# Kernel tuning notes

Measured on AMD Instinct MI355X. Metric: run time of the kernel, lower is better.

## Reference

```python
import jax, jax.numpy as jnp
import numpy as np

N, INSIZE, K, D = 512, 512, 64, 16


def setup_inputs() -> dict:
    key = jax.random.key(0)
    k1, k2, k3 = jax.random.split(key, 3)
    x = jax.random.normal(k1, (N, INSIZE), dtype=jnp.float32)
    W = jax.random.normal(k2, (K * D, INSIZE), dtype=jnp.float32) * (1.0 / np.sqrt(INSIZE))
    b = jax.random.normal(k3, (K * D,), dtype=jnp.float32) * 0.01
    return {"x": x, "W": W, "b": b}


def reference(x, W, b):
    # Linear: [N, insize] -> [N, K*D] -> [N, K, D]
    feat = (x @ W.T + b).reshape(-1, K, D)
    n = feat.shape[0]
    # Pairwise L1 distance over D: norm[i, k, j] = sum_d |feat[i,k,d] - feat[j,k,d]|
    # feature [N,K,D,1] vs feature_ [1,K,D,N] in the original broadcast
    diff = jnp.abs(feat[:, :, :, None] - jnp.transpose(feat, (1, 2, 0))[None])  # [N,K,D,N]
    norm = jnp.sum(diff, axis=2)  # [N,K,N]
    # Eraser: suppress self-similarity on the diagonal with a large penalty
    eraser = jnp.eye(n, dtype=feat.dtype)[:, None, :]  # [N,1,N]
    c_b = jnp.exp(-(norm + eraser * 1e6))
    o_b = jnp.sum(c_b, axis=2)  # [N,K]
    return jnp.concatenate((x, o_b), axis=1)  # [N, insize+K]
```

## Files before the change

### kernel.cpp

```cpp
#include <hip/hip_runtime.h>

#define NPTS 512
#define INS  512
#define KDIM 64
#define DDIM 16
#define CDIM (KDIM*DDIM)
#define OUTC (INS + KDIM)

typedef __attribute__((ext_vector_type(4))) float f32x4;
typedef __attribute__((ext_vector_type(8))) short short8v;
typedef __attribute__((ext_vector_type(4))) unsigned short u16x4;
typedef __attribute__((ext_vector_type(8))) unsigned short u16x8;

__device__ __forceinline__ float exp2_fast(float x) {
    return __builtin_amdgcn_exp2f(x);
}

__device__ __forceinline__ unsigned short f2bf_rne(float f) {
    unsigned u = __float_as_uint(f);
    u += 0x7FFF + ((u >> 16) & 1);
    return (unsigned short)(u >> 16);
}
__device__ __forceinline__ float bf2f(unsigned short h) {
    return __uint_as_float(((unsigned)h) << 16);
}

__global__ __launch_bounds__(256) void convert_kernel(
    const float* __restrict__ x, const float* __restrict__ W,
    float* __restrict__ out,
    unsigned short* __restrict__ xh, unsigned short* __restrict__ xl,
    unsigned short* __restrict__ wh, unsigned short* __restrict__ wl)
{
    const int b = blockIdx.x;
    const int tid = threadIdx.x;
    if (b < 768) {
        const int gid = b * 256 + tid;
        const float4* src;
        unsigned short *dh, *dl;
        int idx;
        if (gid < NPTS * INS / 4) {
            src = (const float4*)x; idx = gid; dh = xh; dl = xl;
        } else {
            src = (const float4*)W; idx = gid - NPTS * INS / 4; dh = wh; dl = wl;
        }
        float4 v = src[idx];
        u16x4 hv, lv;
        hv[0] = f2bf_rne(v.x); lv[0] = f2bf_rne(v.x - bf2f(hv[0]));
        hv[1] = f2bf_rne(v.y); lv[1] = f2bf_rne(v.y - bf2f(hv[1]));
        hv[2] = f2bf_rne(v.z); lv[2] = f2bf_rne(v.z - bf2f(hv[2]));
        hv[3] = f2bf_rne(v.w); lv[3] = f2bf_rne(v.w - bf2f(hv[3]));
        *(u16x4*)&dh[idx * 4] = hv;
        *(u16x4*)&dl[idx * 4] = lv;
    } else {
        const int idx = (b - 768) * 256 + tid;
        const int i  = idx >> 7;
        const int j4 = idx & 127;
        ((float4*)out)[i * (OUTC / 4) + j4] = ((const float4*)x)[i * (INS / 4) + j4];
    }
}

#define BM 32
#define BN 64
#define BK 32
#define LDK 40

__global__ __launch_bounds__(256) void gemm_mfma_kernel(
    const unsigned short* __restrict__ xh, const unsigned short* __restrict__ xl,
    const unsigned short* __restrict__ wh, const unsigned short* __restrict__ wl,
    const float* __restrict__ bias,
    float* __restrict__ featT)
{
    __shared__ unsigned short Ah[BM * LDK], Al[BM * LDK];
    __shared__ unsigned short Bh[BN * LDK], Bl[BN * LDK];

    const int tid   = threadIdx.x;
    const int cbase = blockIdx.x * BN;
    const int ibase = blockIdx.y * BM;

    const int lane = tid & 63;
    const int wv   = tid >> 6;
    const int wm   = wv >> 1;
    const int wn   = wv & 1;

    const int arow = (tid & 127) >> 2;
    const int brow = tid >> 2;
    const int kg   = tid & 3;
    const bool doA = (tid < 128);
    const size_t gA0 = (size_t)(ibase + arow) * INS + kg * 8;
    const size_t gB0 = (size_t)(cbase + brow) * INS + kg * 8;
    const int aloff = arow * LDK + kg * 8;
    const int bloff = brow * LDK + kg * 8;

    const int frow = lane & 15;
    const int fg   = lane >> 4;
    const int aoff = (wm * 16 + frow) * LDK + fg * 8;
    const int boff = (wn * 32 + frow) * LDK + fg * 8;

    f32x4 acc[2] = {};

    u16x8 rah, ral, rbh, rbl;
    if (doA) { rah = *(const u16x8*)&xh[gA0]; ral = *(const u16x8*)&xl[gA0]; }
    rbh = *(const u16x8*)&wh[gB0];
    rbl = *(const u16x8*)&wl[gB0];

    for (int kt = 0; kt < INS / BK; ++kt) {
        __syncthreads();
        if (doA) { *(u16x8*)&Ah[aloff] = rah; *(u16x8*)&Al[aloff] = ral; }
        *(u16x8*)&Bh[bloff] = rbh;
        *(u16x8*)&Bl[bloff] = rbl;
        __syncthreads();
        if (kt + 1 < INS / BK) {
            const size_t o = (size_t)(kt + 1) * BK;
            if (doA) { rah = *(const u16x8*)&xh[gA0 + o]; ral = *(const u16x8*)&xl[gA0 + o]; }
            rbh = *(const u16x8*)&wh[gB0 + o];
            rbl = *(const u16x8*)&wl[gB0 + o];
        }

        short8v av_h = *(const short8v*)&Ah[aoff];
        short8v av_l = *(const short8v*)&Al[aoff];
        #pragma unroll
        for (int n = 0; n < 2; ++n) {
            short8v bv_h = *(const short8v*)&Bh[boff + n * 16 * LDK];
            short8v bv_l = *(const short8v*)&Bl[boff + n * 16 * LDK];
            acc[n] = __builtin_amdgcn_mfma_f32_16x16x32_bf16(av_h, bv_h, acc[n], 0, 0, 0);
            acc[n] = __builtin_amdgcn_mfma_f32_16x16x32_bf16(av_h, bv_l, acc[n], 0, 0, 0);
            acc[n] = __builtin_amdgcn_mfma_f32_16x16x32_bf16(av_l, bv_h, acc[n], 0, 0, 0);
        }
    }

    const float LOG2E = 1.4426950408889634f;
    const int r0 = (lane >> 4) * 4;
    const int i0 = ibase + wm * 16 + r0;
    #pragma unroll
    for (int n = 0; n < 2; ++n) {
        const int c  = cbase + wn * 32 + n * 16 + (lane & 15);
        const float bv = bias[c];
        const int kk = c >> 4;
        const int d  = c & 15;
        float* dst = featT + (size_t)kk * NPTS * DDIM + d;
        #pragma unroll
        for (int r = 0; r < 4; ++r) {
            dst[(size_t)(i0 + r) * DDIM] = (acc[n][r] + bv) * LOG2E;
        }
    }
}

__global__ __launch_bounds__(1024, 4) void pairwise_kernel(
    const float* __restrict__ f, float* __restrict__ out)
{
    const int k     = blockIdx.x;
    const int itile = blockIdx.y;

    __shared__ float part[16][128];

    const int tid  = threadIdx.x;
    const int lane = tid & 63;
    const int wv   = __builtin_amdgcn_readfirstlane(tid >> 6);
    const int i0   = itile * 128 + lane;
    const int i1   = i0 + 64;

    float fi0[16], fi1[16];
    {
        const float4* p0 = (const float4*)(f + ((size_t)k * NPTS + i0) * DDIM);
        const float4* p1 = (const float4*)(f + ((size_t)k * NPTS + i1) * DDIM);
        #pragma unroll
        for (int q = 0; q < 4; ++q) {
            float4 a = p0[q];
            fi0[q * 4 + 0] = a.x; fi0[q * 4 + 1] = a.y;
            fi0[q * 4 + 2] = a.z; fi0[q * 4 + 3] = a.w;
            float4 b = p1[q];
            fi1[q * 4 + 0] = b.x; fi1[q * 4 + 1] = b.y;
            fi1[q * 4 + 2] = b.z; fi1[q * 4 + 3] = b.w;
        }
    }

    const float* __restrict__ jrow = f + ((size_t)k * NPTS + wv * 32) * DDIM;

    float acc0 = 0.f, acc1 = 0.f;
    #pragma unroll 2
    for (int jj = 0; jj < 32; ++jj) {
        const float* p = jrow + jj * DDIM;
        float4 q0 = *(const float4*)(p);
        float4 q1 = *(const float4*)(p + 4);
        float4 q2 = *(const float4*)(p + 8);
        float4 q3 = *(const float4*)(p + 12);
        {
            float a0 = fabsf(fi0[0]  - q0.x) + fabsf(fi0[1]  - q0.y)
                     + fabsf(fi0[2]  - q0.z) + fabsf(fi0[3]  - q0.w);
            float a1 = fabsf(fi0[4]  - q1.x) + fabsf(fi0[5]  - q1.y)
                     + fabsf(fi0[6]  - q1.z) + fabsf(fi0[7]  - q1.w);
            float a2 = fabsf(fi0[8]  - q2.x) + fabsf(fi0[9]  - q2.y)
                     + fabsf(fi0[10] - q2.z) + fabsf(fi0[11] - q2.w);
            float a3 = fabsf(fi0[12] - q3.x) + fabsf(fi0[13] - q3.y)
                     + fabsf(fi0[14] - q3.z) + fabsf(fi0[15] - q3.w);
            acc0 += exp2_fast(-((a0 + a1) + (a2 + a3)));
        }
        {
            float b0 = fabsf(fi1[0]  - q0.x) + fabsf(fi1[1]  - q0.y)
                     + fabsf(fi1[2]  - q0.z) + fabsf(fi1[3]  - q0.w);
            float b1 = fabsf(fi1[4]  - q1.x) + fabsf(fi1[5]  - q1.y)
                     + fabsf(fi1[6]  - q1.z) + fabsf(fi1[7]  - q1.w);
            float b2 = fabsf(fi1[8]  - q2.x) + fabsf(fi1[9]  - q2.y)
                     + fabsf(fi1[10] - q2.z) + fabsf(fi1[11] - q2.w);
            float b3 = fabsf(fi1[12] - q3.x) + fabsf(fi1[13] - q3.y)
                     + fabsf(fi1[14] - q3.z) + fabsf(fi1[15] - q3.w);
            acc1 += exp2_fast(-((b0 + b1) + (b2 + b3)));
        }
    }

    part[wv][lane]      = acc0;
    part[wv][lane + 64] = acc1;
    __syncthreads();

    if (tid < 128) {
        float s = (((part[0][tid]  + part[1][tid])  + (part[2][tid]  + part[3][tid]))
                +  ((part[4][tid]  + part[5][tid])  + (part[6][tid]  + part[7][tid])))
                + (((part[8][tid]  + part[9][tid])  + (part[10][tid] + part[11][tid]))
                +  ((part[12][tid] + part[13][tid]) + (part[14][tid] + part[15][tid])));
        const int i = itile * 128 + tid;
        out[(size_t)i * OUTC + INS + k] = s - 1.0f;
    }
}

extern "C" void kernel_launch(void* const* d_in, const int* in_sizes, int n_in,
                              void* d_out, int out_size, void* d_ws, size_t ws_size,
                              hipStream_t stream) {
    const float* x    = (const float*)d_in[0];
    const float* W    = (const float*)d_in[1];
    const float* bias = (const float*)d_in[2];
    float* out = (float*)d_out;

    float* featT = (float*)d_ws;
    unsigned short* xh = (unsigned short*)((char*)d_ws + (size_t)(2 << 20));
    unsigned short* xl = xh + (size_t)NPTS * INS;
    unsigned short* wh = xl + (size_t)NPTS * INS;
    unsigned short* wl = wh + (size_t)CDIM * INS;

    convert_kernel<<<dim3(1024), 256, 0, stream>>>(x, W, out, xh, xl, wh, wl);
    gemm_mfma_kernel<<<dim3(CDIM / BN, NPTS / BM), 256, 0, stream>>>(
        xh, xl, wh, wl, bias, featT);
    pairwise_kernel<<<dim3(KDIM, 4), 1024, 0, stream>>>(featT, out);
}
```

Baseline: 91.25 us.

## Exploit pairwise distance symmetry with triangular tiles and atomic accumulation

The pairwise L1 kernel now computes only the upper-triangular 128x128 tile pairs (10 tiles per k instead of 16), using the symmetry of the distance matrix. Off-diagonal tiles also reduce column sums through wave shuffles and add them to the transposed rows. Results are accumulated with atomicAdd into an output column that convert_kernel first initialises to -1. This cuts the exp and abs work by roughly 40%, in exchange for atomics, extra shuffle reductions and smaller blocks, and summation order now varies between runs.

```diff
diff --git a/kernel.cpp b/kernel.cpp
--- a/kernel.cpp
+++ b/kernel.cpp
@@ -51,11 +51,17 @@
         hv[3] = f2bf_rne(v.w); lv[3] = f2bf_rne(v.w - bf2f(hv[3]));
         *(u16x4*)&dh[idx * 4] = hv;
         *(u16x4*)&dl[idx * 4] = lv;
-    } else {
+    } else if (b < 1024) {
         const int idx = (b - 768) * 256 + tid;
         const int i  = idx >> 7;
         const int j4 = idx & 127;
         ((float4*)out)[i * (OUTC / 4) + j4] = ((const float4*)x)[i * (INS / 4) + j4];
+    } else {
+        const int idx = (b - 1024) * 256 + tid;
+        const int i  = idx >> 4;
+        const int c4 = idx & 15;
+        ((float4*)out)[i * (OUTC / 4) + INS / 4 + c4] =
+            make_float4(-1.0f, -1.0f, -1.0f, -1.0f);
     }
 }
 
@@ -145,18 +151,22 @@
     }
 }
 
-__global__ __launch_bounds__(1024, 4) void pairwise_kernel(
+__global__ __launch_bounds__(512) void pairwise_kernel(
     const float* __restrict__ f, float* __restrict__ out)
 {
-    const int k     = blockIdx.x;
-    const int itile = blockIdx.y;
-
-    __shared__ float part[16][128];
+    const int k  = blockIdx.x;
+    const int tz = blockIdx.y;
+    const int ti = (int)((0x2110003210ULL >> (4 * tz)) & 0xF);
+    const int tj = (int)((0x3323213210ULL >> (4 * tz)) & 0xF);
+    const bool offdiag = (tz >= 4);
+
+    __shared__ float part[8][128];
+    __shared__ float colLds[128];
 
     const int tid  = threadIdx.x;
     const int lane = tid & 63;
     const int wv   = __builtin_amdgcn_readfirstlane(tid >> 6);
-    const int i0   = itile * 128 + lane;
+    const int i0   = ti * 128 + lane;
     const int i1   = i0 + 64;
 
     float fi0[16], fi1[16];
@@ -174,16 +184,18 @@
         }
     }
 
-    const float* __restrict__ jrow = f + ((size_t)k * NPTS + wv * 32) * DDIM;
+    const float* __restrict__ jrow = f + ((size_t)k * NPTS + tj * 128 + wv * 16) * DDIM;
 
     float acc0 = 0.f, acc1 = 0.f;
-    #pragma unroll 2
-    for (int jj = 0; jj < 32; ++jj) {
+    float colacc[16];
+    #pragma unroll
+    for (int jj = 0; jj < 16; ++jj) {
         const float* p = jrow + jj * DDIM;
         float4 q0 = *(const float4*)(p);
         float4 q1 = *(const float4*)(p + 4);
         float4 q2 = *(const float4*)(p + 8);
         float4 q3 = *(const float4*)(p + 12);
+        float e0, e1;
         {
             float a0 = fabsf(fi0[0]  - q0.x) + fabsf(fi0[1]  - q0.y)
                      + fabsf(fi0[2]  - q0.z) + fabsf(fi0[3]  - q0.w);
@@ -193,7 +205,7 @@
                      + fabsf(fi0[10] - q2.z) + fabsf(fi0[11] - q2.w);
             float a3 = fabsf(fi0[12] - q3.x) + fabsf(fi0[13] - q3.y)
                      + fabsf(fi0[14] - q3.z) + fabsf(fi0[15] - q3.w);
-            acc0 += exp2_fast(-((a0 + a1) + (a2 + a3)));
+            e0 = exp2_fast(-((a0 + a1) + (a2 + a3)));
         }
         {
             float b0 = fabsf(fi1[0]  - q0.x) + fabsf(fi1[1]  - q0.y)
@@ -204,21 +216,36 @@
                      + fabsf(fi1[10] - q2.z) + fabsf(fi1[11] - q2.w);
             float b3 = fabsf(fi1[12] - q3.x) + fabsf(fi1[13] - q3.y)
                      + fabsf(fi1[14] - q3.z) + fabsf(fi1[15] - q3.w);
-            acc1 += exp2_fast(-((b0 + b1) + (b2 + b3)));
-        }
-    }
-
+            e1 = exp2_fast(-((b0 + b1) + (b2 + b3)));
+        }
+        acc0 += e0;
+        acc1 += e1;
+        colacc[jj] = e0 + e1;
+    }
+
+    if (offdiag) {
+        #pragma unroll
+        for (int jj = 0; jj < 16; ++jj) {
+            float s = colacc[jj];
+            s += __shfl_xor(s, 32);
+            s += __shfl_xor(s, 16);
+            s += __shfl_xor(s, 8);
+            s += __shfl_xor(s, 4);
+            s += __shfl_xor(s, 2);
+            s += __shfl_xor(s, 1);
+            if (lane == 0) colLds[wv * 16 + jj] = s;
+        }
+    }
     part[wv][lane]      = acc0;
     part[wv][lane + 64] = acc1;
     __syncthreads();
 
     if (tid < 128) {
-        float s = (((part[0][tid]  + part[1][tid])  + (part[2][tid]  + part[3][tid]))
-                +  ((part[4][tid]  + part[5][tid])  + (part[6][tid]  + part[7][tid])))
-                + (((part[8][tid]  + part[9][tid])  + (part[10][tid] + part[11][tid]))
-                +  ((part[12][tid] + part[13][tid]) + (part[14][tid] + part[15][tid])));
-        const int i = itile * 128 + tid;
-        out[(size_t)i * OUTC + INS + k] = s - 1.0f;
+        float s = ((part[0][tid] + part[1][tid]) + (part[2][tid] + part[3][tid]))
+                + ((part[4][tid] + part[5][tid]) + (part[6][tid] + part[7][tid]));
+        atomicAdd(&out[(size_t)(ti * 128 + tid) * OUTC + INS + k], s);
+        if (offdiag)
+            atomicAdd(&out[(size_t)(tj * 128 + tid) * OUTC + INS + k], colLds[tid]);
     }
 }
 
@@ -236,8 +263,8 @@
     unsigned short* wh = xl + (size_t)NPTS * INS;
     unsigned short* wl = wh + (size_t)CDIM * INS;
 
-    convert_kernel<<<dim3(1024), 256, 0, stream>>>(x, W, out, xh, xl, wh, wl);
+    convert_kernel<<<dim3(1056), 256, 0, stream>>>(x, W, out, xh, xl, wh, wl);
     gemm_mfma_kernel<<<dim3(CDIM / BN, NPTS / BM), 256, 0, stream>>>(
         xh, xl, wh, wl, bias, featT);
-    pairwise_kernel<<<dim3(KDIM, 4), 1024, 0, stream>>>(featT, out);
-}
+    pairwise_kernel<<<dim3(KDIM, 10), 512, 0, stream>>>(featT, out);
+}
```

Result: no change. 90.08 us (-1.3%).
